# Optimization experiments

Measured on AMD Instinct MI355X. Metric: run time of the kernel, lower is better.

## Reference

```python
import jax, jax.numpy as jnp
import numpy as np

D, H, O, N = 1024, 4096, 1024, 8
T = float(np.e)
NA = max(1, int(N * 0.7))  # 5 active experts

def setup_inputs() -> dict:
    key = jax.random.key(0)
    ks = jax.random.split(key, 7)
    s = lambda fan_in: 1.0 / np.sqrt(fan_in)
    x  = jax.random.normal(ks[0], (4096, D), dtype=jnp.float32)
    W1 = jax.random.uniform(ks[1], (N, H, D), jnp.float32, -s(D), s(D))
    b1 = jax.random.uniform(ks[2], (N, H),    jnp.float32, -s(D), s(D))
    W2 = jax.random.uniform(ks[3], (N, O, H), jnp.float32, -s(H), s(H))
    b2 = jax.random.uniform(ks[4], (N, O),    jnp.float32, -s(H), s(H))
    Wg = jax.random.uniform(ks[5], (N, D),    jnp.float32, -s(D), s(D))
    bg = jax.random.uniform(ks[6], (N,),      jnp.float32, -s(D), s(D))
    return {"x": x, "W1": W1, "b1": b1, "W2": W2, "b2": b2, "Wg": Wg, "bg": bg}

def reference(x, W1, b1, W2, b2, Wg, bg):
    # All-expert dense FFN: eo[b,n,o]
    hpre = jnp.einsum('bd,nhd->bnh', x, W1) + b1  # [B,N,H]
    hact = jax.nn.relu(hpre)
    eo = jnp.einsum('bnh,noh->bno', hact, W2) + b2  # [B,N,O]
    # Boltzmann gate
    logits = x @ Wg.T + bg                      # [B,N]
    p = jax.nn.softmax(logits / T, axis=-1)
    _, idx = jax.lax.top_k(p, NA)               # [B,NA]
    rows = jnp.arange(p.shape[0])[:, None]
    m = jnp.zeros_like(p).at[rows, idx].set(1.0)
    w = p * m
    w = w / (w.sum(-1, keepdims=True) + 1e-8)
    return jnp.einsum('bn,bno->bo', w, eo)
```

## Files before the change

### kernel.cpp

```cpp
#include <hip/hip_runtime.h>
#include <stdint.h>


#define B_TOK 4096
#define DD 1024
#define HH 4096
#define OO 1024
#define NE 8
#define NA_K 5

typedef __attribute__((ext_vector_type(8))) __bf16 bf16x8;
typedef __attribute__((ext_vector_type(4))) float f32x4;

__device__ __forceinline__ unsigned short f2bf(float f) {
  unsigned u = __float_as_uint(f);
  u += 0x7FFF + ((u >> 16) & 1);
  return (unsigned short)(u >> 16);
}

__device__ __forceinline__ void gload_lds16(const void* g, void* l) {
  __builtin_amdgcn_global_load_lds(
      (const __attribute__((address_space(1))) void*)g,
      (__attribute__((address_space(3))) void*)l, 16, 0, 0);
}

__global__ void moe_cvt_kernel(const float* __restrict__ src,
                               unsigned short* __restrict__ dst, int count4) {
  int i = blockIdx.x * blockDim.x + threadIdx.x;
  const int stride = gridDim.x * blockDim.x;
  for (; i < count4; i += stride) {
    const float4 v = ((const float4*)src)[i];
    ushort4 o;
    o.x = f2bf(v.x); o.y = f2bf(v.y); o.z = f2bf(v.z); o.w = f2bf(v.w);
    ((ushort4*)dst)[i] = o;
  }
}

__global__ __launch_bounds__(256) void moe_gate_kernel(
    const float* __restrict__ x, const float* __restrict__ Wg,
    const float* __restrict__ bg, float* __restrict__ gatew) {
  const int b = blockIdx.x;
  const int t = threadIdx.x;
  const float4 xv = ((const float4*)(x + (size_t)b * DD))[t];
  float part[NE];
#pragma unroll
  for (int n = 0; n < NE; ++n) {
    const float4 wv = ((const float4*)(Wg + (size_t)n * DD))[t];
    part[n] = xv.x * wv.x + xv.y * wv.y + xv.z * wv.z + xv.w * wv.w;
  }
#pragma unroll
  for (int n = 0; n < NE; ++n)
#pragma unroll
    for (int off = 32; off > 0; off >>= 1)
      part[n] += __shfl_down(part[n], off);
  __shared__ float red[4][NE];
  const int l = t & 63, w = t >> 6;
  if (l == 0) {
#pragma unroll
    for (int n = 0; n < NE; ++n) red[w][n] = part[n];
  }
  __syncthreads();
  if (t == 0) {
    float lg[NE];
#pragma unroll
    for (int n = 0; n < NE; ++n)
      lg[n] = red[0][n] + red[1][n] + red[2][n] + red[3][n] + bg[n];
    float mx = lg[0];
#pragma unroll
    for (int n = 1; n < NE; ++n) mx = fmaxf(mx, lg[n]);
    const float invT = 0.36787944117144233f;
    float p[NE], s = 0.0f;
#pragma unroll
    for (int n = 0; n < NE; ++n) { p[n] = expf((lg[n] - mx) * invT); s += p[n]; }
#pragma unroll
    for (int n = 0; n < NE; ++n) p[n] /= s;
    bool sel[NE];
#pragma unroll
    for (int n = 0; n < NE; ++n) sel[n] = false;
    float ssum = 0.0f;
    for (int k2 = 0; k2 < NA_K; ++k2) {
      int best = -1; float bv = -1e30f;
      for (int n = 0; n < NE; ++n)
        if (!sel[n] && p[n] > bv) { bv = p[n]; best = n; }
      sel[best] = true; ssum += p[best];
    }
    const float inv = 1.0f / (ssum + 1e-8f);
#pragma unroll
    for (int n = 0; n < NE; ++n)
      gatew[(size_t)b * NE + n] = sel[n] ? p[n] * inv : 0.0f;
  }
}

__global__ __launch_bounds__(256, 2) void moe_ffn1_kernel(
    const unsigned short* __restrict__ xbf,
    const unsigned short* __restrict__ W1bf,
    const float* __restrict__ b1,
    const float* __restrict__ gatew,
    unsigned short* __restrict__ H1s) {
  const int n  = blockIdx.z;
  const int tm = blockIdx.y * 128;
  const int tn = blockIdx.x * 128;
  const int t  = threadIdx.x;
  const int l  = t & 63;
  const int w  = t >> 6;
  const int wr = w >> 1, wc = w & 1;
  const int lrow = l & 15, lk = l >> 4;

  __shared__ __align__(16) unsigned short lds_a[128 * 32];
  __shared__ __align__(16) unsigned short lds_b[128 * 32];

  const unsigned short* Abase = xbf + (size_t)tm * DD;
  const unsigned short* Bbase = W1bf + ((size_t)n * HH + tn) * DD;

  f32x4 acc[4][4] = {};

  char* la = (char*)lds_a + w * 1024;
  char* lb = (char*)lds_b + w * 1024;
  const int r0 = t >> 2;
  const int cb = (t & 3) * 8;

  for (int kk = 0; kk < DD / 32; ++kk) {
    const unsigned short* Ak = Abase + kk * 32 + cb;
    const unsigned short* Bk = Bbase + kk * 32 + cb;
    gload_lds16(Ak + (size_t)r0 * DD, la);
    gload_lds16(Ak + (size_t)(r0 + 64) * DD, la + 4096);
    gload_lds16(Bk + (size_t)r0 * DD, lb);
    gload_lds16(Bk + (size_t)(r0 + 64) * DD, lb + 4096);
    __syncthreads();
    bf16x8 af[4], bfr[4];
#pragma unroll
    for (int i = 0; i < 4; ++i)
      af[i] = *(const bf16x8*)((const char*)lds_a + (wr * 64 + i * 16 + lrow) * 64 + lk * 16);
#pragma unroll
    for (int j = 0; j < 4; ++j)
      bfr[j] = *(const bf16x8*)((const char*)lds_b + (wc * 64 + j * 16 + lrow) * 64 + lk * 16);
#pragma unroll
    for (int i = 0; i < 4; ++i)
#pragma unroll
      for (int j = 0; j < 4; ++j)
        acc[i][j] = __builtin_amdgcn_mfma_f32_16x16x32_bf16(af[i], bfr[j], acc[i][j], 0, 0, 0);
    __syncthreads();
  }

#pragma unroll
  for (int i = 0; i < 4; ++i) {
#pragma unroll
    for (int r = 0; r < 4; ++r) {
      const int row = tm + wr * 64 + i * 16 + lk * 4 + r;
      const float gw = gatew[(size_t)row * NE + n];
#pragma unroll
      for (int j = 0; j < 4; ++j) {
        const int col = tn + wc * 64 + j * 16 + lrow;
        float v = acc[i][j][r] + b1[(size_t)n * HH + col];
        v = fmaxf(v, 0.0f) * gw;
        H1s[((size_t)n * B_TOK + row) * HH + col] = f2bf(v);
      }
    }
  }
}

__global__ __launch_bounds__(256, 2) void moe_ffn2_kernel(
    const unsigned short* __restrict__ H1s,
    const unsigned short* __restrict__ W2bf,
    float* __restrict__ part) {
  const int zp = blockIdx.z;
  const int tm = blockIdx.y * 128;
  const int tn = blockIdx.x * 128;
  const int t  = threadIdx.x;
  const int l  = t & 63;
  const int w  = t >> 6;
  const int wr = w >> 1, wc = w & 1;
  const int lrow = l & 15, lk = l >> 4;

  __shared__ __align__(16) unsigned short lds_a[128 * 32];
  __shared__ __align__(16) unsigned short lds_b[128 * 32];

  f32x4 acc[4][4] = {};

  char* la = (char*)lds_a + w * 1024;
  char* lb = (char*)lds_b + w * 1024;
  const int r0 = t >> 2;
  const int cb = (t & 3) * 8;

  for (int n = zp * 4; n < zp * 4 + 4; ++n) {
    const unsigned short* Abase = H1s + ((size_t)n * B_TOK + tm) * HH;
    const unsigned short* Bbase = W2bf + ((size_t)n * OO + tn) * HH;
    for (int kk = 0; kk < HH / 32; ++kk) {
      const unsigned short* Ak = Abase + kk * 32 + cb;
      const unsigned short* Bk = Bbase + kk * 32 + cb;
      gload_lds16(Ak + (size_t)r0 * HH, la);
      gload_lds16(Ak + (size_t)(r0 + 64) * HH, la + 4096);
      gload_lds16(Bk + (size_t)r0 * HH, lb);
      gload_lds16(Bk + (size_t)(r0 + 64) * HH, lb + 4096);
      __syncthreads();
      bf16x8 af[4], bfr[4];
#pragma unroll
      for (int i = 0; i < 4; ++i)
        af[i] = *(const bf16x8*)((const char*)lds_a + (wr * 64 + i * 16 + lrow) * 64 + lk * 16);
#pragma unroll
      for (int j = 0; j < 4; ++j)
        bfr[j] = *(const bf16x8*)((const char*)lds_b + (wc * 64 + j * 16 + lrow) * 64 + lk * 16);
#pragma unroll
      for (int i = 0; i < 4; ++i)
#pragma unroll
        for (int j = 0; j < 4; ++j)
          acc[i][j] = __builtin_amdgcn_mfma_f32_16x16x32_bf16(af[i], bfr[j], acc[i][j], 0, 0, 0);
      __syncthreads();
    }
  }

  float* pout = part + (size_t)zp * B_TOK * OO;
#pragma unroll
  for (int i = 0; i < 4; ++i) {
#pragma unroll
    for (int r = 0; r < 4; ++r) {
      const int row = tm + wr * 64 + i * 16 + lk * 4 + r;
#pragma unroll
      for (int j = 0; j < 4; ++j) {
        const int col = tn + wc * 64 + j * 16 + lrow;
        pout[(size_t)row * OO + col] = acc[i][j][r];
      }
    }
  }
}

__global__ void moe_finalize_kernel(const float* __restrict__ part,
                                    const float* __restrict__ gatew,
                                    const float* __restrict__ b2,
                                    float* __restrict__ out) {
  const int e4 = blockIdx.x * blockDim.x + threadIdx.x;
  if (e4 >= B_TOK * OO / 4) return;
  const int b  = e4 >> 8;
  const int o4 = e4 & 255;
  const float4 p0 = ((const float4*)part)[e4];
  const float4 p1 = ((const float4*)(part + (size_t)B_TOK * OO))[e4];
  float sx = p0.x + p1.x, sy = p0.y + p1.y, sz = p0.z + p1.z, sw = p0.w + p1.w;
#pragma unroll
  for (int n = 0; n < NE; ++n) {
    const float gw = gatew[(size_t)b * NE + n];
    const float4 bb = ((const float4*)(b2 + (size_t)n * OO))[o4];
    sx += gw * bb.x; sy += gw * bb.y; sz += gw * bb.z; sw += gw * bb.w;
  }
  float4 r; r.x = sx; r.y = sy; r.z = sz; r.w = sw;
  ((float4*)out)[e4] = r;
}

extern "C" void kernel_launch(void* const* d_in, const int* in_sizes, int n_in,
                              void* d_out, int out_size, void* d_ws, size_t ws_size,
                              hipStream_t stream) {
  const float* x  = (const float*)d_in[0];
  const float* W1 = (const float*)d_in[1];
  const float* b1 = (const float*)d_in[2];
  const float* W2 = (const float*)d_in[3];
  const float* b2 = (const float*)d_in[4];
  const float* Wg = (const float*)d_in[5];
  const float* bg = (const float*)d_in[6];
  float* out = (float*)d_out;

  char* ws = (char*)d_ws;
  unsigned short* xbf   = (unsigned short*)(ws);
  unsigned short* W1bf  = (unsigned short*)(ws + (size_t)(8u)  * (1u << 20));
  unsigned short* W2bf  = (unsigned short*)(ws + (size_t)(72u) * (1u << 20));
  float*          gatew = (float*)(ws + (size_t)(136u) * (1u << 20));
  unsigned short* H1s   = (unsigned short*)(ws + (size_t)(138u) * (1u << 20));
  float*          part  = (float*)(ws + (size_t)(394u) * (1u << 20));

  moe_cvt_kernel<<<2048, 256, 0, stream>>>(x, xbf, B_TOK * DD / 4);
  moe_cvt_kernel<<<2048, 256, 0, stream>>>(W1, W1bf, NE * HH * DD / 4);
  moe_cvt_kernel<<<2048, 256, 0, stream>>>(W2, W2bf, NE * OO * HH / 4);
  moe_gate_kernel<<<B_TOK, 256, 0, stream>>>(x, Wg, bg, gatew);
  moe_ffn1_kernel<<<dim3(HH / 128, B_TOK / 128, NE), 256, 0, stream>>>(xbf, W1bf, b1, gatew, H1s);
  moe_ffn2_kernel<<<dim3(OO / 128, B_TOK / 128, 2), 256, 0, stream>>>(H1s, W2bf, part);
  moe_finalize_kernel<<<(B_TOK * OO / 4) / 256, 256, 0, stream>>>(part, gatew, b2, out);
}
```

Before: 1.204 ms.

## Remap GEMM workgroups across XCDs and raise FFN2 split-K to four partitions

Both FFN GEMM kernels move to a 1D grid whose block index is remapped so that consecutive logical tiles land on the same XCD (block id mod 8 interleave), aiming for better L2 reuse of the A/B tiles. FFN2's expert split grows from 2 to 4 partitions of 2 experts each, doubling the grid to 1024 workgroups for better CU fill, and finalize now sums four partial buffers. Launch bounds are raised to 4 waves per SIMD, and the workspace is relaid out so the partial buffers reuse the W1 bf16 region after FFN1 finishes. The extra partials add write and read traffic in finalize, and the higher occupancy target may constrain register allocation.

Measured after the change: 1.004 ms. 1.2x faster.

```diff
diff --git a/kernel.cpp b/kernel.cpp
--- a/kernel.cpp
+++ b/kernel.cpp
@@ -91,15 +91,17 @@
   }
 }
 
-__global__ __launch_bounds__(256, 2) void moe_ffn1_kernel(
+__global__ __launch_bounds__(256, 4) void moe_ffn1_kernel(
     const unsigned short* __restrict__ xbf,
     const unsigned short* __restrict__ W1bf,
     const float* __restrict__ b1,
     const float* __restrict__ gatew,
     unsigned short* __restrict__ H1s) {
-  const int n  = blockIdx.z;
-  const int tm = blockIdx.y * 128;
-  const int tn = blockIdx.x * 128;
+  const int nwg = 8192;
+  const int lid = (blockIdx.x % 8) * (nwg / 8) + (blockIdx.x / 8);
+  const int tn = (lid & 31) * 128;
+  const int tm = ((lid >> 5) & 31) * 128;
+  const int n  = lid >> 10;
   const int t  = threadIdx.x;
   const int l  = t & 63;
   const int w  = t >> 6;
@@ -159,13 +161,15 @@
   }
 }
 
-__global__ __launch_bounds__(256, 2) void moe_ffn2_kernel(
+__global__ __launch_bounds__(256, 4) void moe_ffn2_kernel(
     const unsigned short* __restrict__ H1s,
     const unsigned short* __restrict__ W2bf,
     float* __restrict__ part) {
-  const int zp = blockIdx.z;
-  const int tm = blockIdx.y * 128;
-  const int tn = blockIdx.x * 128;
+  const int nwg = 1024;
+  const int lid = (blockIdx.x % 8) * (nwg / 8) + (blockIdx.x / 8);
+  const int tn = (lid & 7) * 128;
+  const int tm = ((lid >> 3) & 31) * 128;
+  const int zp = lid >> 8;
   const int t  = threadIdx.x;
   const int l  = t & 63;
   const int w  = t >> 6;
@@ -182,7 +186,7 @@
   const int r0 = t >> 2;
   const int cb = (t & 3) * 8;
 
-  for (int n = zp * 4; n < zp * 4 + 4; ++n) {
+  for (int n = zp * 2; n < zp * 2 + 2; ++n) {
     const unsigned short* Abase = H1s + ((size_t)n * B_TOK + tm) * HH;
     const unsigned short* Bbase = W2bf + ((size_t)n * OO + tn) * HH;
     for (int kk = 0; kk < HH / 32; ++kk) {
@@ -232,9 +236,12 @@
   if (e4 >= B_TOK * OO / 4) return;
   const int b  = e4 >> 8;
   const int o4 = e4 & 255;
-  const float4 p0 = ((const float4*)part)[e4];
-  const float4 p1 = ((const float4*)(part + (size_t)B_TOK * OO))[e4];
-  float sx = p0.x + p1.x, sy = p0.y + p1.y, sz = p0.z + p1.z, sw = p0.w + p1.w;
+  float sx = 0.f, sy = 0.f, sz = 0.f, sw = 0.f;
+#pragma unroll
+  for (int z = 0; z < 4; ++z) {
+    const float4 p = ((const float4*)(part + (size_t)z * B_TOK * OO))[e4];
+    sx += p.x; sy += p.y; sz += p.z; sw += p.w;
+  }
 #pragma unroll
   for (int n = 0; n < NE; ++n) {
     const float gw = gatew[(size_t)b * NE + n];
@@ -257,19 +264,20 @@
   const float* bg = (const float*)d_in[6];
   float* out = (float*)d_out;
 
+  const size_t MB = 1u << 20;
   char* ws = (char*)d_ws;
   unsigned short* xbf   = (unsigned short*)(ws);
-  unsigned short* W1bf  = (unsigned short*)(ws + (size_t)(8u)  * (1u << 20));
-  unsigned short* W2bf  = (unsigned short*)(ws + (size_t)(72u) * (1u << 20));
-  float*          gatew = (float*)(ws + (size_t)(136u) * (1u << 20));
-  unsigned short* H1s   = (unsigned short*)(ws + (size_t)(138u) * (1u << 20));
-  float*          part  = (float*)(ws + (size_t)(394u) * (1u << 20));
+  float*          gatew = (float*)(ws + 8 * MB);
+  unsigned short* W2bf  = (unsigned short*)(ws + 10 * MB);
+  unsigned short* H1s   = (unsigned short*)(ws + 74 * MB);
+  unsigned short* W1bf  = (unsigned short*)(ws + 330 * MB);
+  float*          part  = (float*)(ws + 330 * MB);
 
   moe_cvt_kernel<<<2048, 256, 0, stream>>>(x, xbf, B_TOK * DD / 4);
   moe_cvt_kernel<<<2048, 256, 0, stream>>>(W1, W1bf, NE * HH * DD / 4);
   moe_cvt_kernel<<<2048, 256, 0, stream>>>(W2, W2bf, NE * OO * HH / 4);
   moe_gate_kernel<<<B_TOK, 256, 0, stream>>>(x, Wg, bg, gatew);
-  moe_ffn1_kernel<<<dim3(HH / 128, B_TOK / 128, NE), 256, 0, stream>>>(xbf, W1bf, b1, gatew, H1s);
-  moe_ffn2_kernel<<<dim3(OO / 128, B_TOK / 128, 2), 256, 0, stream>>>(H1s, W2bf, part);
-  moe_finalize_kernel<<<(B_TOK * OO / 4) / 256, 256, 0, stream>>>(part, gatew, b2, out);
-}
+  moe_ffn1_kernel<<<8192, 256, 0, stream>>>(xbf, W1bf, b1, gatew, H1s);
+  moe_ffn2_kernel<<<1024, 256, 0, stream>>>(H1s, W2bf, part);
+  moe_finalize_kernel<<<(B_TOK * OO / 4 + 255) / 256, 256, 0, stream>>>(part, gatew, b2, out);
+}
```
